# Kernel tuning notes

Measured on AMD Instinct MI355X. Metric: run time of the kernel, lower is better.

The kernel has to match this reference:

```python
import jax, jax.numpy as jnp
import numpy as np

EPS = 1e-5  # torch BatchNorm2d default eps (eval mode with running stats)


def bn(x, g, b, m, v):
    # x: [B,C,H,W]; per-channel affine batchnorm in inference form
    return (x - m[:, None, None]) * (g[:, None, None] / jnp.sqrt(v[:, None, None] + EPS)) + b[:, None, None]


def self_attn(x, Wq, bq, Wk, bk, Wv, bv, rel_h, rel_w):
    # x: [B,C,H,W]; Wq/Wk/Wv: [C,C] (1x1 convs); rel_h: [C,H]; rel_w: [C,W]
    B, C, H, W = x.shape
    N = H * W
    q = jnp.einsum('oc,bchw->bohw', Wq, x).reshape(B, C, N) + bq[None, :, None]
    k = jnp.einsum('oc,bchw->bohw', Wk, x).reshape(B, C, N) + bk[None, :, None]
    v = jnp.einsum('oc,bchw->bohw', Wv, x).reshape(B, C, N) + bv[None, :, None]
    energy = jnp.einsum('bcn,bcm->bnm', q, k)                      # content: Q^T K
    pos = (rel_h[:, :, None] + rel_w[:, None, :]).reshape(C, N)    # [C, H*W]
    energy = energy + jnp.einsum('bcn,cm->bnm', q, pos)            # rel-pos bias term
    attn = jax.nn.softmax(energy, axis=-1)                         # [B,N,N]
    out = jnp.einsum('bcm,bnm->bcn', v, attn)                      # V @ attn^T
    return out.reshape(B, C, H, W)


def conv3x3(x, w):
    return jax.lax.conv_general_dilated(x, w, (1, 1), 'SAME',
                                        dimension_numbers=('NCHW', 'OIHW', 'NCHW'))


def setup_inputs() -> dict:
    key = jax.random.key(0)
    B, C, H, W, NH = 32, 512, 16, 16, 5
    ks = jax.random.split(key, 32)
    f = lambda i, shape, s=1.0: jax.random.normal(ks[i], shape, jnp.float32) * s
    inp = {
        'x0': f(0, (B, C, H, W)), 'x1': f(1, (B, C, H, W)), 'x2': f(2, (B, C, H, W)),
        'x3': f(3, (B, C, H, W)), 'x': f(4, (B, C, H, W)),
        'qW': f(5, (NH, C, C), 0.02), 'qB': f(6, (NH, C), 0.02),
        'kW': f(7, (NH, C, C), 0.02), 'kB': f(8, (NH, C), 0.02),
        'vW': f(9, (NH, C, C), 0.02), 'vB': f(10, (NH, C), 0.02),
        'relH': f(11, (NH, C, H)), 'relW': f(12, (NH, C, W)),
        'msw_W': f(13, (NH - 1, NH * C), 0.02),
        'msw_g': jnp.ones((NH - 1,)), 'msw_b': jnp.zeros((NH - 1,)),
        'msw_m': jnp.zeros((NH - 1,)), 'msw_v': jnp.ones((NH - 1,)),
        'fus_W': f(14, (C, C, 3, 3), 0.02),
        'fus_g': jnp.ones((C,)), 'fus_b': jnp.zeros((C,)),
        'fus_m': jnp.zeros((C,)), 'fus_v': jnp.ones((C,)),
        'top_g': jnp.ones((C,)), 'top_b': jnp.zeros((C,)),
        'top_m': jnp.zeros((C,)), 'top_v': jnp.ones((C,)),
        'h': 16, 'w': 16,
    }
    return inp


def reference(x0, x1, x2, x3, x, qW, qB, kW, kB, vW, vB, relH, relW,
              msw_W, msw_g, msw_b, msw_m, msw_v,
              fus_W, fus_g, fus_b, fus_m, fus_v,
              top_g, top_b, top_m, top_v, h, w):
    B, C, H, W = x.shape
    xs = jnp.stack([x0, x1, x2, x3, x])                            # [5,B,C,H,W]
    outs = jax.vmap(self_attn)(xs, qW, qB, kW, kB, vW, vB, relH, relW)  # [5,B,C,H,W]
    cat = outs.transpose(1, 0, 2, 3, 4).reshape(B, 5 * C, H, W)
    weights = jax.nn.sigmoid(bn(jnp.einsum('oc,bchw->bohw', msw_W, cat),
                                msw_g, msw_b, msw_m, msw_v))        # [B,4,H,W]
    x_ms = (weights[:, 0:1] * outs[0] + weights[:, 1:2] * outs[1]
            + weights[:, 2:3] * outs[2] + weights[:, 3:4] * outs[3] + outs[4])
    x_ms = jax.nn.relu(bn(conv3x3(x_ms, fus_W), fus_g, fus_b, fus_m, fus_v))
    out = jax.nn.relu(bn(x_ms + x, top_g, top_b, top_m, top_v))
    return out
```

## Files before the change

### kernel.cpp

```cpp
#include <hip/hip_runtime.h>
#include <cstdint>

using bf16x8  = __attribute__((ext_vector_type(8))) __bf16;
using f32x4   = __attribute__((ext_vector_type(4))) float;
using ushort8 = __attribute__((ext_vector_type(8))) unsigned short;

#define EPSN 1e-5f

__device__ __forceinline__ void gld16(const void* g, void* l) {
  __builtin_amdgcn_global_load_lds((const __attribute__((address_space(1))) void*)g,
                                   (__attribute__((address_space(3))) void*)l, 16, 0, 0);
}

__device__ __forceinline__ ushort f2bf(float f) {
  __bf16 h = (__bf16)f;
  return __builtin_bit_cast(unsigned short, h);
}
__device__ __forceinline__ float bf2f(ushort u) {
  union { uint32_t u; float f; } v; v.u = ((uint32_t)u) << 16; return v.f;
}

__device__ __forceinline__ void gemm_core(const ushort* __restrict__ Ag,
                                          const ushort* __restrict__ Bg,
                                          int ldk, int ksteps,
                                          ushort* As, ushort* Bs,
                                          f32x4 (&acc)[4][4]) {
  const int t = threadIdx.x, lane = t & 63, w = t >> 6;
  const int wr = w >> 1, wc = w & 1;
  for (int kt = 0; kt < ksteps; ++kt) {
    const int kbase = kt * 64;
#pragma unroll
    for (int p = 0; p < 4; ++p) {
      int q = p * 256 + t;
      int row = q >> 3, slot = q & 7;
      int srcs = slot ^ (row & 7);
      gld16(Ag + (size_t)row * ldk + kbase + srcs * 8, As + (p * 256 + w * 64) * 8);
      gld16(Bg + (size_t)row * ldk + kbase + srcs * 8, Bs + (p * 256 + w * 64) * 8);
    }
    __syncthreads();
#pragma unroll
    for (int kk = 0; kk < 2; ++kk) {
      bf16x8 af[4], bfv[4];
#pragma unroll
      for (int i = 0; i < 4; ++i) {
        int ra = wr * 64 + i * 16 + (lane & 15);
        int sa = (kk * 4 + (lane >> 4)) ^ (ra & 7);
        af[i] = *(const bf16x8*)(As + ra * 64 + sa * 8);
        int rb = wc * 64 + i * 16 + (lane & 15);
        int sb = (kk * 4 + (lane >> 4)) ^ (rb & 7);
        bfv[i] = *(const bf16x8*)(Bs + rb * 64 + sb * 8);
      }
#pragma unroll
      for (int i = 0; i < 4; ++i)
#pragma unroll
        for (int j = 0; j < 4; ++j)
          acc[i][j] = __builtin_amdgcn_mfma_f32_16x16x32_bf16(af[i], bfv[j], acc[i][j], 0, 0, 0);
    }
    __syncthreads();
  }
}

__global__ __launch_bounds__(256) void k_pre(const float* __restrict__ x0,
                                             const float* __restrict__ x1,
                                             const float* __restrict__ x2,
                                             const float* __restrict__ x3,
                                             const float* __restrict__ x4,
                                             const float* __restrict__ qW,
                                             const float* __restrict__ kW,
                                             const float* __restrict__ vW,
                                             const float* __restrict__ relH,
                                             const float* __restrict__ relW,
                                             ushort* __restrict__ xT,
                                             ushort* __restrict__ Wb,
                                             ushort* __restrict__ posb) {
  __shared__ float tile[64][65];
  int bid = blockIdx.x;
  const int t = threadIdx.x;
  if (bid < 5120) {
    const int nt4 = bid & 3;  bid >>= 2;
    const int ct  = bid & 7;  bid >>= 3;
    const int b   = bid & 31; bid >>= 5;
    const int ix  = bid;
    const float* xs = ix == 0 ? x0 : ix == 1 ? x1 : ix == 2 ? x2 : ix == 3 ? x3 : x4;
    const float* src = xs + ((size_t)b * 512 + ct * 64) * 256 + nt4 * 64;
    const int col = t & 63, rq = t >> 6;
#pragma unroll
    for (int rr = 0; rr < 16; ++rr) {
      int row = rr * 4 + rq;
      tile[row][col] = src[(size_t)row * 256 + col];
    }
    __syncthreads();
    ushort* dst = xT + ((size_t)(ix * 32 + b) * 256 + nt4 * 64) * 512 + ct * 64;
#pragma unroll
    for (int rr = 0; rr < 16; ++rr) {
      int nrow = rr * 4 + rq;
      dst[(size_t)nrow * 512 + col] = f2bf(tile[col][nrow]);
    }
  } else if (bid < 8960) {
    int idx = (bid - 5120) * 256 + t;
    int gi = idx * 4;
    int sel = gi / 1310720;
    int off = gi - sel * 1310720;
    const float* src = sel == 0 ? qW : (sel == 1 ? kW : vW);
    float4 vv = *(const float4*)(src + off);
    int h = off / 262144, rest = off - h * 262144;
    ushort4 o;
    o.x = f2bf(vv.x); o.y = f2bf(vv.y); o.z = f2bf(vv.z); o.w = f2bf(vv.w);
    *(ushort4*)(Wb + (size_t)(h * 3 + sel) * 262144 + rest) = o;
  } else {
    int idx8 = (bid - 8960) * 256 + t;
    int e0 = idx8 * 8;
    int c0 = e0 & 511, m = (e0 >> 9) & 255, h = e0 >> 17;
    ushort8 o;
#pragma unroll
    for (int e = 0; e < 8; ++e) {
      int c = c0 + e;
      o[e] = f2bf(relH[((size_t)h * 512 + c) * 16 + (m >> 4)] +
                  relW[((size_t)h * 512 + c) * 16 + (m & 15)]);
    }
    *(ushort8*)(posb + e0) = o;
  }
}

__global__ __launch_bounds__(512, 4) void k_qkv3(const ushort* __restrict__ Wb,
                                                 const ushort* __restrict__ xT,
                                                 const ushort* __restrict__ posb,
                                                 const float* __restrict__ qB,
                                                 const float* __restrict__ kB,
                                                 const float* __restrict__ vB,
                                                 ushort* __restrict__ qT,
                                                 ushort* __restrict__ kpT,
                                                 ushort* __restrict__ vv) {
  extern __shared__ ushort ls[];
  const int t = threadIdx.x, lane = t & 63;
  const int w = t >> 6, wm = w >> 2, wn = w & 3, g = lane >> 4, l = lane & 15;
  int bid = blockIdx.x;
  bid = (bid & 7) * 240 + (bid >> 3);
  const int h = bid / 384;
  const int r = bid % 384;

  const ushort* Ag;
  const ushort* Bg;
  const bool partA = r < 256;
  int pt = 0, nt = 0, mt = 0, ntv = 0;
  if (partA) {
    pt = r >> 2; nt = r & 3;
    Ag = xT + ((size_t)h * 8192 + pt * 128) * 512;
    Bg = Wb + ((size_t)(h * 3 + (nt >> 1)) * 512 + (nt & 1) * 256) * 512;
  } else {
    const int r2 = r - 256;
    mt = r2 >> 5; ntv = r2 & 31;
    Ag = Wb + ((size_t)(h * 3 + 2) * 512 + mt * 128) * 512;
    Bg = xT + ((size_t)h * 8192 + ntv * 256) * 512;
  }

  f32x4 acc[4][4];
#pragma unroll
  for (int i = 0; i < 4; ++i)
#pragma unroll
    for (int j = 0; j < 4; ++j) acc[i][j] = f32x4{0.f, 0.f, 0.f, 0.f};

#define QKV_STAGE(tt, slot)                                                    \
  {                                                                            \
    const int kb_ = (tt) * 32;                                                 \
    ushort* sa_ = ls + (slot) * 4096;                                          \
    ushort* sb_ = ls + 8192 + (slot) * 8192;                                   \
    {                                                                          \
      int q_ = t;                                                              \
      int row_ = q_ >> 2, s4_ = q_ & 3;                                        \
      int src_ = s4_ ^ ((row_ ^ (row_ >> 2)) & 3);                             \
      gld16(Ag + (size_t)row_ * 512 + kb_ + src_ * 8, sa_ + q_ * 8);           \
    }                                                                          \
    _Pragma("unroll")                                                          \
    for (int p_ = 0; p_ < 2; ++p_) {                                           \
      int q_ = p_ * 512 + t;                                                   \
      int row_ = q_ >> 2, s4_ = q_ & 3;                                        \
      int src_ = s4_ ^ ((row_ ^ (row_ >> 2)) & 3);                             \
      gld16(Bg + (size_t)row_ * 512 + kb_ + src_ * 8, sb_ + q_ * 8);           \
    }                                                                          \
  }

#define QKV_COMPUTE(slot)                                                      \
  {                                                                            \
    ushort* sa_ = ls + (slot) * 4096;                                          \
    ushort* sb_ = ls + 8192 + (slot) * 8192;                                   \
    bf16x8 af[4], bfv[4];                                                      \
    _Pragma("unroll")                                                          \
    for (int j_ = 0; j_ < 4; ++j_) {                                           \
      int rb_ = wn * 64 + j_ * 16 + l;                                         \
      int sb2_ = g ^ ((rb_ ^ (rb_ >> 2)) & 3);                                 \
      bfv[j_] = *(const bf16x8*)(sb_ + rb_ * 32 + sb2_ * 8);                   \
    }                                                                          \
    _Pragma("unroll")                                                          \
    for (int i_ = 0; i_ < 4; ++i_) {                                           \
      int ra_ = wm * 64 + i_ * 16 + l;                                         \
      int sa2_ = g ^ ((ra_ ^ (ra_ >> 2)) & 3);                                 \
      af[i_] = *(const bf16x8*)(sa_ + ra_ * 32 + sa2_ * 8);                    \
    }                                                                          \
    asm volatile("s_waitcnt lgkmcnt(0)" ::: "memory");                         \
    __builtin_amdgcn_sched_barrier(0);                                         \
    __builtin_amdgcn_s_setprio(1);                                             \
    _Pragma("unroll")                                                          \
    for (int i_ = 0; i_ < 4; ++i_)                                             \
      _Pragma("unroll")                                                        \
      for (int j_ = 0; j_ < 4; ++j_)                                           \
        acc[i_][j_] = __builtin_amdgcn_mfma_f32_16x16x32_bf16(af[i_], bfv[j_], \
                                                              acc[i_][j_], 0, 0, 0); \
    __builtin_amdgcn_s_setprio(0);                                             \
  }

  QKV_STAGE(0, 0);
  for (int tt = 0; tt < 15; ++tt) {
    __builtin_amdgcn_s_barrier();
    QKV_STAGE(tt + 1, (tt + 1) & 1);
    __builtin_amdgcn_sched_barrier(0);
    asm volatile("s_waitcnt vmcnt(3)" ::: "memory");
    __builtin_amdgcn_s_barrier();
    __builtin_amdgcn_sched_barrier(0);
    QKV_COMPUTE(tt & 1);
  }
  __builtin_amdgcn_sched_barrier(0);
  asm volatile("s_waitcnt vmcnt(0)" ::: "memory");
  __builtin_amdgcn_s_barrier();
  __builtin_amdgcn_sched_barrier(0);
  QKV_COMPUTE(1);
  __syncthreads();

  ushort(*Cs)[260] = (ushort(*)[260])ls;
  if (partA) {
    const bool isq = nt < 2;
    const float* bias = (isq ? qB : kB) + (size_t)h * 512 + (nt & 1) * 256;
    ushort* dst = isq ? qT : kpT;
    float bj[4];
#pragma unroll
    for (int j = 0; j < 4; ++j) bj[j] = bias[wn * 64 + j * 16 + l];
#pragma unroll
    for (int R = 0; R < 2; ++R) {
      if (wm == R) {
#pragma unroll
        for (int i = 0; i < 4; ++i)
#pragma unroll
          for (int j = 0; j < 4; ++j)
#pragma unroll
            for (int rr = 0; rr < 4; ++rr)
              Cs[i * 16 + g * 4 + rr][wn * 64 + j * 16 + l] = f2bf(acc[i][j][rr] + bj[j]);
      }
      __syncthreads();
#pragma unroll
      for (int it = 0; it < 4; ++it) {
        int lin = it * 512 + t;
        int row = lin >> 5, cc8 = (lin & 31) * 8;
        int pglob = pt * 128 + R * 64 + row;
        ushort8 cv = *(const ushort8*)&Cs[row][cc8];
        if (!isq) {
          ushort8 pv = *(const ushort8*)(posb + ((size_t)h * 256 + (pglob & 255)) * 512 +
                                         (nt & 1) * 256 + cc8);
#pragma unroll
          for (int e = 0; e < 8; ++e) cv[e] = f2bf(bf2f(cv[e]) + bf2f(pv[e]));
        }
        *(ushort8*)(dst + ((size_t)h * 8192 + pglob) * 512 + (nt & 1) * 256 + cc8) = cv;
      }
      if (R == 0) __syncthreads();
    }
  } else {
    const float* bias = vB + (size_t)h * 512 + mt * 128;
#pragma unroll
    for (int R = 0; R < 2; ++R) {
      if (wm == R) {
#pragma unroll
        for (int i = 0; i < 4; ++i) {
          float4 b4 = *(const float4*)(bias + R * 64 + i * 16 + g * 4);
#pragma unroll
          for (int j = 0; j < 4; ++j)
#pragma unroll
            for (int rr = 0; rr < 4; ++rr)
              Cs[i * 16 + g * 4 + rr][wn * 64 + j * 16 + l] =
                  f2bf(acc[i][j][rr] + ((const float*)&b4)[rr]);
        }
      }
      __syncthreads();
#pragma unroll
      for (int it = 0; it < 4; ++it) {
        int lin = it * 512 + t;
        int row = lin >> 5, cc8 = (lin & 31) * 8;
        int og = mt * 128 + R * 64 + row;
        ushort8 cv = *(const ushort8*)&Cs[row][cc8];
        *(ushort8*)(vv + (((size_t)(h * 32 + ntv)) * 512 + og) * 256 + cc8) = cv;
      }
      if (R == 0) __syncthreads();
    }
  }
#undef QKV_STAGE
#undef QKV_COMPUTE
}

__global__ __launch_bounds__(256) void k_attn(const ushort* __restrict__ qT,
                                              const ushort* __restrict__ kpT,
                                              const float* __restrict__ fusW,
                                              ushort* __restrict__ attn,
                                              ushort* __restrict__ Wconv) {
  __shared__ ushort sm[20480];
  __shared__ float red[4][64];
  __shared__ float comb[64];
  int bid = blockIdx.x;
  const int t = threadIdx.x;
  if (bid >= 640) {
    int p = (bid - 640) * 256 + t;
    const float* src = fusW + (size_t)p * 9;
    float vv[9];
#pragma unroll
    for (int s = 0; s < 9; ++s) vv[s] = src[s];
#pragma unroll
    for (int s = 0; s < 9; ++s) Wconv[(size_t)s * 262144 + p] = f2bf(vv[s]);
    return;
  }
  bid = (bid & 7) * 80 + (bid >> 3);
  const int rt = bid & 3;
  const int hb = bid >> 2;
  ushort* As = sm;
  ushort* Bs = sm + 4096;
  const ushort* Ag = qT + ((size_t)hb * 256 + rt * 64) * 512;
  const ushort* Bg = kpT + (size_t)hb * 256 * 512;
  const int lane = t & 63, w = t >> 6, g = lane >> 4, l = lane & 15;

  f32x4 acc[4][4];
#pragma unroll
  for (int i = 0; i < 4; ++i)
#pragma unroll
    for (int j = 0; j < 4; ++j) acc[i][j] = f32x4{0.f, 0.f, 0.f, 0.f};

  for (int kt = 0; kt < 8; ++kt) {
    const int kbase = kt * 64;
#pragma unroll
    for (int p = 0; p < 2; ++p) {
      int q = p * 256 + t;
      int row = q >> 3, slot = q & 7, srcs = slot ^ (row & 7);
      gld16(Ag + (size_t)row * 512 + kbase + srcs * 8, As + (p * 256 + w * 64) * 8);
    }
#pragma unroll
    for (int p = 0; p < 8; ++p) {
      int q = p * 256 + t;
      int row = q >> 3, slot = q & 7, srcs = slot ^ (row & 7);
      gld16(Bg + (size_t)row * 512 + kbase + srcs * 8, Bs + (p * 256 + w * 64) * 8);
    }
    __syncthreads();
#pragma unroll
    for (int kk = 0; kk < 2; ++kk) {
      bf16x8 af[4], bfv[4];
#pragma unroll
      for (int i = 0; i < 4; ++i) {
        int ra = i * 16 + l;
        int sa = (kk * 4 + g) ^ (ra & 7);
        af[i] = *(const bf16x8*)(As + ra * 64 + sa * 8);
        int rb = w * 64 + i * 16 + l;
        int sb = (kk * 4 + g) ^ (rb & 7);
        bfv[i] = *(const bf16x8*)(Bs + rb * 64 + sb * 8);
      }
#pragma unroll
      for (int i = 0; i < 4; ++i)
#pragma unroll
        for (int j = 0; j < 4; ++j)
          acc[i][j] = __builtin_amdgcn_mfma_f32_16x16x32_bf16(af[i], bfv[j], acc[i][j], 0, 0, 0);
    }
    __syncthreads();
  }

#pragma unroll
  for (int i = 0; i < 4; ++i)
#pragma unroll
    for (int rr = 0; rr < 4; ++rr) {
      float v = fmaxf(fmaxf(acc[i][0][rr], acc[i][1][rr]), fmaxf(acc[i][2][rr], acc[i][3][rr]));
#pragma unroll
      for (int m = 1; m < 16; m <<= 1) v = fmaxf(v, __shfl_xor(v, m));
      if (l == 0) red[w][i * 16 + g * 4 + rr] = v;
    }
  __syncthreads();
  if (t < 64) comb[t] = fmaxf(fmaxf(red[0][t], red[1][t]), fmaxf(red[2][t], red[3][t]));
  __syncthreads();
#pragma unroll
  for (int i = 0; i < 4; ++i)
#pragma unroll
    for (int rr = 0; rr < 4; ++rr) {
      float mx = comb[i * 16 + g * 4 + rr];
      float s = 0.f;
#pragma unroll
      for (int j = 0; j < 4; ++j) {
        float e = expf(acc[i][j][rr] - mx);
        acc[i][j][rr] = e;
        s += e;
      }
#pragma unroll
      for (int m = 1; m < 16; m <<= 1) s += __shfl_xor(s, m);
      if (l == 0) red[w][i * 16 + g * 4 + rr] = s;
    }
  __syncthreads();
  if (t < 64) comb[t] = red[0][t] + red[1][t] + red[2][t] + red[3][t];
  __syncthreads();
  ushort(*P)[260] = (ushort(*)[260])sm;
#pragma unroll
  for (int i = 0; i < 4; ++i)
#pragma unroll
    for (int rr = 0; rr < 4; ++rr) {
      int row = i * 16 + g * 4 + rr;
      float inv = 1.f / comb[row];
#pragma unroll
      for (int j = 0; j < 4; ++j)
        P[row][w * 64 + j * 16 + l] = f2bf(acc[i][j][rr] * inv);
    }
  __syncthreads();
  ushort* Arow = attn + (size_t)hb * 65536 + (size_t)rt * 16384;
#pragma unroll
  for (int it = 0; it < 8; ++it) {
    int lin = it * 256 + t;
    int row = lin >> 5, c8 = (lin & 31) * 8;
    ushort8 cv = *(const ushort8*)&P[row][c8];
    *(ushort8*)(Arow + (size_t)row * 256 + c8) = cv;
  }
}

__global__ __launch_bounds__(256) void k_pv(const ushort* __restrict__ attn,
                                            const ushort* __restrict__ vv,
                                            ushort* __restrict__ OT) {
  __shared__ ushort lds[128 * 148];
  ushort* As = lds;
  ushort* Bs = lds + 8192;
  int bid = blockIdx.x;
  bid = (bid & 7) * 160 + (bid >> 3);
  const int nt = bid & 3; bid >>= 2;
  const int mt = bid & 1; bid >>= 1;
  const size_t hb = (size_t)bid;
  const ushort* Ag = attn + (hb * 256 + mt * 128) * 256;
  const ushort* Bg = vv + (hb * 512 + nt * 128) * 256;
  f32x4 acc[4][4];
#pragma unroll
  for (int i = 0; i < 4; ++i)
#pragma unroll
    for (int j = 0; j < 4; ++j) acc[i][j] = f32x4{0.f, 0.f, 0.f, 0.f};
  gemm_core(Ag, Bg, 256, 4, As, Bs, acc);
  const int t = threadIdx.x, lane = t & 63, w = t >> 6;
  const int wr = w >> 1, wc = w & 1, g = lane >> 4, l = lane & 15;
  ushort(*Cs)[148] = (ushort(*)[148])lds;
#pragma unroll
  for (int i = 0; i < 4; ++i)
#pragma unroll
    for (int j = 0; j < 4; ++j)
#pragma unroll
      for (int rr = 0; rr < 4; ++rr)
        Cs[wr * 64 + i * 16 + g * 4 + rr][wc * 64 + j * 16 + l] = f2bf(acc[i][j][rr]);
  __syncthreads();
#pragma unroll
  for (int it = 0; it < 8; ++it) {
    int lin = it * 256 + t;
    int row = lin >> 4, cc = (lin & 15) * 8;
    ushort8 cv = *(const ushort8*)&Cs[row][cc];
    *(ushort8*)(OT + (hb * 256 + mt * 128 + row) * 512 + nt * 128 + cc) = cv;
  }
}

__global__ __launch_bounds__(256) void k_weights(const ushort* __restrict__ OT,
                                                 const float* __restrict__ mswW,
                                                 const float* __restrict__ mg,
                                                 const float* __restrict__ mb,
                                                 const float* __restrict__ mm,
                                                 const float* __restrict__ mv,
                                                 ushort* __restrict__ xmsT) {
  __shared__ float msw[10240];
  const int t = threadIdx.x, lane = t & 63, w = t >> 6;
#pragma unroll
  for (int it = 0; it < 10; ++it) {
    int idx = it * 1024 + t * 4;
    *(float4*)(msw + idx) = *(const float4*)(mswW + idx);
  }
  __syncthreads();
  const size_t pix = (size_t)blockIdx.x * 4 + w;
  float o[5][2][4];
#pragma unroll
  for (int h = 0; h < 5; ++h)
#pragma unroll
    for (int hf = 0; hf < 2; ++hf) {
      ushort4 v = *(const ushort4*)(OT + ((size_t)h * 8192 + pix) * 512 + hf * 256 + lane * 4);
      o[h][hf][0] = bf2f(v.x); o[h][hf][1] = bf2f(v.y);
      o[h][hf][2] = bf2f(v.z); o[h][hf][3] = bf2f(v.w);
    }
  float a[4] = {0.f, 0.f, 0.f, 0.f};
#pragma unroll
  for (int j = 0; j < 4; ++j)
#pragma unroll
    for (int h = 0; h < 5; ++h)
#pragma unroll
      for (int hf = 0; hf < 2; ++hf) {
        float4 m4 = *(const float4*)(msw + j * 2560 + h * 512 + hf * 256 + lane * 4);
        a[j] += m4.x * o[h][hf][0] + m4.y * o[h][hf][1] +
                m4.z * o[h][hf][2] + m4.w * o[h][hf][3];
      }
#pragma unroll
  for (int m = 1; m < 64; m <<= 1) {
    a[0] += __shfl_xor(a[0], m); a[1] += __shfl_xor(a[1], m);
    a[2] += __shfl_xor(a[2], m); a[3] += __shfl_xor(a[3], m);
  }
  float wj[4];
#pragma unroll
  for (int j = 0; j < 4; ++j) {
    float val = (a[j] - mm[j]) * (mg[j] * rsqrtf(mv[j] + EPSN)) + mb[j];
    wj[j] = 1.f / (1.f + expf(-val));
  }
#pragma unroll
  for (int hf = 0; hf < 2; ++hf) {
    float r0 = wj[0] * o[0][hf][0] + wj[1] * o[1][hf][0] + wj[2] * o[2][hf][0] + wj[3] * o[3][hf][0] + o[4][hf][0];
    float r1 = wj[0] * o[0][hf][1] + wj[1] * o[1][hf][1] + wj[2] * o[2][hf][1] + wj[3] * o[3][hf][1] + o[4][hf][1];
    float r2 = wj[0] * o[0][hf][2] + wj[1] * o[1][hf][2] + wj[2] * o[2][hf][2] + wj[3] * o[3][hf][2] + o[4][hf][2];
    float r3 = wj[0] * o[0][hf][3] + wj[1] * o[1][hf][3] + wj[2] * o[2][hf][3] + wj[3] * o[3][hf][3] + o[4][hf][3];
    ushort4 pk; pk.x = f2bf(r0); pk.y = f2bf(r1); pk.z = f2bf(r2); pk.w = f2bf(r3);
    *(ushort4*)(xmsT + pix * 512 + hf * 256 + lane * 4) = pk;
  }
}

__global__ __launch_bounds__(256) void k_conv(const ushort* __restrict__ Wconv,
                                              const ushort* __restrict__ xmsT,
                                              float* __restrict__ y1a,
                                              float* __restrict__ y1b) {
  __shared__ ushort As3[3 * 128 * 64];
  __shared__ ushort xp[180 * 76];
  int bid = blockIdx.x;
  bid = (bid & 7) * 64 + (bid >> 3);
  const int ntl = bid & 1; bid >>= 1;
  const int mt = bid & 3;  bid >>= 2;
  const int halfk = bid & 1; bid >>= 1;
  const int bb = bid;
  const int y0 = ntl * 8;
  const int t = threadIdx.x, lane = t & 63, w = t >> 6, wr = w >> 1, wc = w & 1;
  f32x4 acc[4][4];
#pragma unroll
  for (int i = 0; i < 4; ++i)
#pragma unroll
    for (int j = 0; j < 4; ++j) acc[i][j] = f32x4{0.f, 0.f, 0.f, 0.f};

  for (int cb = halfk * 4; cb < halfk * 4 + 4; ++cb) {
    __syncthreads();
    for (int u = t; u < 1440; u += 256) {
      int slot = u & 7;
      int xpi = (u >> 3) % 18;
      int rl = u / 144;
      int yg = y0 - 1 + rl, xg = xpi - 1;
      uint4 val = make_uint4(0, 0, 0, 0);
      if (yg >= 0 && yg < 16 && (unsigned)xg < 16u)
        val = *(const uint4*)(xmsT + ((size_t)bb * 256 + yg * 16 + xg) * 512 + cb * 64 + slot * 8);
      *(uint4*)(xp + (rl * 18 + xpi) * 76 + slot * 8) = val;
    }
    for (int dy = 0; dy < 3; ++dy) {
#pragma unroll
      for (int dx = 0; dx < 3; ++dx)
#pragma unroll
        for (int p = 0; p < 4; ++p) {
          int q = p * 256 + t;
          int row = q >> 3, slot = q & 7, srcs = slot ^ (row & 7);
          gld16(Wconv + ((size_t)(dy * 3 + dx) * 512 + mt * 128 + row) * 512 + cb * 64 + srcs * 8,
                As3 + dx * 8192 + (p * 256 + w * 64) * 8);
        }
      __syncthreads();
#pragma unroll
      for (int dx = 0; dx < 3; ++dx)
#pragma unroll
        for (int kk = 0; kk < 2; ++kk) {
          bf16x8 af[4], bfv[4];
#pragma unroll
          for (int i = 0; i < 4; ++i) {
            int ra = wr * 64 + i * 16 + (lane & 15);
            int sa = (kk * 4 + (lane >> 4)) ^ (ra & 7);
            af[i] = *(const bf16x8*)(As3 + dx * 8192 + ra * 64 + sa * 8);
            int nl = wc * 64 + i * 16 + (lane & 15);
            int pp = ((nl >> 4) + dy) * 18 + (nl & 15) + dx;
            bfv[i] = *(const bf16x8*)(xp + pp * 76 + (kk * 4 + (lane >> 4)) * 8);
          }
#pragma unroll
          for (int i = 0; i < 4; ++i)
#pragma unroll
            for (int j = 0; j < 4; ++j)
              acc[i][j] = __builtin_amdgcn_mfma_f32_16x16x32_bf16(af[i], bfv[j], acc[i][j], 0, 0, 0);
        }
      __syncthreads();
    }
  }
  float* yp = halfk ? y1b : y1a;
  const int o0 = mt * 128 + wr * 64 + ((lane >> 4) << 2);
  const int n0 = ntl * 128 + wc * 64 + (lane & 15);
#pragma unroll
  for (int i = 0; i < 4; ++i)
#pragma unroll
    for (int j = 0; j < 4; ++j)
#pragma unroll
      for (int rr = 0; rr < 4; ++rr) {
        int o = o0 + i * 16 + rr, n = n0 + j * 16;
        yp[((size_t)bb * 512 + o) * 256 + n] = acc[i][j][rr];
      }
}

__global__ __launch_bounds__(256) void k_top(const float* __restrict__ y1a,
                                             const float* __restrict__ y1b,
                                             const float* __restrict__ x,
                                             const float* __restrict__ fg,
                                             const float* __restrict__ fb,
                                             const float* __restrict__ fm,
                                             const float* __restrict__ fv,
                                             const float* __restrict__ tg,
                                             const float* __restrict__ tb,
                                             const float* __restrict__ tm,
                                             const float* __restrict__ tv,
                                             float* __restrict__ out) {
  size_t i4 = ((size_t)blockIdx.x * 256 + threadIdx.x) * 4;
  int c = (int)((i4 >> 8) & 511);
  float4 a = *(const float4*)(y1a + i4);
  float4 bq = *(const float4*)(y1b + i4);
  float4 xx = *(const float4*)(x + i4);
  float sf = fg[c] * rsqrtf(fv[c] + EPSN), mf = fm[c], bf_ = fb[c];
  float st = tg[c] * rsqrtf(tv[c] + EPSN), mt_ = tm[c], bt_ = tb[c];
  float4 o;
  float v;
  v = fmaxf((a.x + bq.x - mf) * sf + bf_, 0.f); o.x = fmaxf((v + xx.x - mt_) * st + bt_, 0.f);
  v = fmaxf((a.y + bq.y - mf) * sf + bf_, 0.f); o.y = fmaxf((v + xx.y - mt_) * st + bt_, 0.f);
  v = fmaxf((a.z + bq.z - mf) * sf + bf_, 0.f); o.z = fmaxf((v + xx.z - mt_) * st + bt_, 0.f);
  v = fmaxf((a.w + bq.w - mf) * sf + bf_, 0.f); o.w = fmaxf((v + xx.w - mt_) * st + bt_, 0.f);
  *(float4*)(out + i4) = o;
}

extern "C" void kernel_launch(void* const* d_in, const int* in_sizes, int n_in,
                              void* d_out, int out_size, void* d_ws, size_t ws_size,
                              hipStream_t stream) {
  const float* x0   = (const float*)d_in[0];
  const float* x1   = (const float*)d_in[1];
  const float* x2   = (const float*)d_in[2];
  const float* x3   = (const float*)d_in[3];
  const float* x4   = (const float*)d_in[4];
  const float* qW   = (const float*)d_in[5];
  const float* qB   = (const float*)d_in[6];
  const float* kW   = (const float*)d_in[7];
  const float* kB   = (const float*)d_in[8];
  const float* vW   = (const float*)d_in[9];
  const float* vB   = (const float*)d_in[10];
  const float* relH = (const float*)d_in[11];
  const float* relW = (const float*)d_in[12];
  const float* mswW = (const float*)d_in[13];
  const float* msg  = (const float*)d_in[14];
  const float* msb  = (const float*)d_in[15];
  const float* msm  = (const float*)d_in[16];
  const float* msv  = (const float*)d_in[17];
  const float* fusW = (const float*)d_in[18];
  const float* fg   = (const float*)d_in[19];
  const float* fb   = (const float*)d_in[20];
  const float* fm   = (const float*)d_in[21];
  const float* fv   = (const float*)d_in[22];
  const float* tg   = (const float*)d_in[23];
  const float* tb   = (const float*)d_in[24];
  const float* tm   = (const float*)d_in[25];
  const float* tv   = (const float*)d_in[26];

  if (ws_size < 180355072ull) return;
  char* ws = (char*)d_ws;
  ushort* xT    = (ushort*)(ws + 0);
  ushort* attn  = (ushort*)(ws + 0);
  ushort* Wconv = (ushort*)(ws + 20971520);
  ushort* qT    = (ushort*)(ws + 41943040);
  ushort* xmsT  = (ushort*)(ws + 41943040);
  float*  y1a   = (float*)(ws + 50331648);
  float*  y1b   = (float*)(ws + 67108864);
  ushort* kpT   = (ushort*)(ws + 83886080);
  ushort* OT    = (ushort*)(ws + 83886080);
  ushort* vv    = (ushort*)(ws + 125829120);
  ushort* Wb    = (ushort*)(ws + 167772160);
  ushort* posb  = (ushort*)(ws + 175636480);

  k_pre    <<<9280, 256, 0, stream>>>(x0, x1, x2, x3, x4, qW, kW, vW, relH, relW,
                                      xT, Wb, posb);
  k_qkv3   <<<1920, 512, 49152, stream>>>(Wb, xT, posb, qB, kB, vB, qT, kpT, vv);
  k_attn   <<<1664, 256, 0, stream>>>(qT, kpT, fusW, attn, Wconv);
  k_pv     <<<1280, 256, 0, stream>>>(attn, vv, OT);
  k_weights<<<2048, 256, 0, stream>>>(OT, mswW, msg, msb, msm, msv, xmsT);
  k_conv   <<<512,  256, 0, stream>>>(Wconv, xmsT, y1a, y1b);
  k_top    <<<4096, 256, 0, stream>>>(y1a, y1b, x4, fg, fb, fm, fv, tg, tb, tm, tv, (float*)d_out);
}
```

Before: 256.1 us.

## Triple-buffer QKV and PV GEMMs, fuse conv epilogue with BN/residual, drop split-K

The QKV GEMM moves from a double-buffered to a triple-buffered LDS pipeline, using more dynamic shared memory and prefetching two stages ahead. The PV GEMM drops the shared synchronous gemm_core for the same triple-buffered pipeline with 32-wide k steps and raised MFMA priority. The 3x3 conv no longer splits K across blocks. It runs with 512 threads and applies both batchnorms, ReLUs and the residual in its epilogue from precomputed per-channel scale/shift, which removes the k_top kernel and the fp32 partial buffers. The trade-off is half as many conv blocks, 256 instead of 512, which may leave compute units idle, plus strided scalar output stores.

Result: faster. 249.0 us (-2.8%).

```diff
diff --git a/kernel.cpp b/kernel.cpp
--- a/kernel.cpp
+++ b/kernel.cpp
@@ -18,46 +18,6 @@
 }
 __device__ __forceinline__ float bf2f(ushort u) {
   union { uint32_t u; float f; } v; v.u = ((uint32_t)u) << 16; return v.f;
-}
-
-__device__ __forceinline__ void gemm_core(const ushort* __restrict__ Ag,
-                                          const ushort* __restrict__ Bg,
-                                          int ldk, int ksteps,
-                                          ushort* As, ushort* Bs,
-                                          f32x4 (&acc)[4][4]) {
-  const int t = threadIdx.x, lane = t & 63, w = t >> 6;
-  const int wr = w >> 1, wc = w & 1;
-  for (int kt = 0; kt < ksteps; ++kt) {
-    const int kbase = kt * 64;
-#pragma unroll
-    for (int p = 0; p < 4; ++p) {
-      int q = p * 256 + t;
-      int row = q >> 3, slot = q & 7;
-      int srcs = slot ^ (row & 7);
-      gld16(Ag + (size_t)row * ldk + kbase + srcs * 8, As + (p * 256 + w * 64) * 8);
-      gld16(Bg + (size_t)row * ldk + kbase + srcs * 8, Bs + (p * 256 + w * 64) * 8);
-    }
-    __syncthreads();
-#pragma unroll
-    for (int kk = 0; kk < 2; ++kk) {
-      bf16x8 af[4], bfv[4];
-#pragma unroll
-      for (int i = 0; i < 4; ++i) {
-        int ra = wr * 64 + i * 16 + (lane & 15);
-        int sa = (kk * 4 + (lane >> 4)) ^ (ra & 7);
-        af[i] = *(const bf16x8*)(As + ra * 64 + sa * 8);
-        int rb = wc * 64 + i * 16 + (lane & 15);
-        int sb = (kk * 4 + (lane >> 4)) ^ (rb & 7);
-        bfv[i] = *(const bf16x8*)(Bs + rb * 64 + sb * 8);
-      }
-#pragma unroll
-      for (int i = 0; i < 4; ++i)
-#pragma unroll
-        for (int j = 0; j < 4; ++j)
-          acc[i][j] = __builtin_amdgcn_mfma_f32_16x16x32_bf16(af[i], bfv[j], acc[i][j], 0, 0, 0);
-    }
-    __syncthreads();
-  }
 }
 
 __global__ __launch_bounds__(256) void k_pre(const float* __restrict__ x0,
@@ -70,9 +30,18 @@
                                              const float* __restrict__ vW,
                                              const float* __restrict__ relH,
                                              const float* __restrict__ relW,
+                                             const float* __restrict__ fg,
+                                             const float* __restrict__ fb,
+                                             const float* __restrict__ fm,
+                                             const float* __restrict__ fv,
+                                             const float* __restrict__ tg,
+                                             const float* __restrict__ tb,
+                                             const float* __restrict__ tm,
+                                             const float* __restrict__ tv,
                                              ushort* __restrict__ xT,
                                              ushort* __restrict__ Wb,
-                                             ushort* __restrict__ posb) {
+                                             ushort* __restrict__ posb,
+                                             float4* __restrict__ bnp) {
   __shared__ float tile[64][65];
   int bid = blockIdx.x;
   const int t = threadIdx.x;
@@ -107,7 +76,7 @@
     ushort4 o;
     o.x = f2bf(vv.x); o.y = f2bf(vv.y); o.z = f2bf(vv.z); o.w = f2bf(vv.w);
     *(ushort4*)(Wb + (size_t)(h * 3 + sel) * 262144 + rest) = o;
-  } else {
+  } else if (bid < 9280) {
     int idx8 = (bid - 8960) * 256 + t;
     int e0 = idx8 * 8;
     int c0 = e0 & 511, m = (e0 >> 9) & 255, h = e0 >> 17;
@@ -119,6 +88,13 @@
                   relW[((size_t)h * 512 + c) * 16 + (m & 15)]);
     }
     *(ushort8*)(posb + e0) = o;
+  } else {
+    int o = (bid - 9280) * 256 + t;
+    float sf = fg[o] * rsqrtf(fv[o] + EPSN);
+    float c1 = fb[o] - fm[o] * sf;
+    float st = tg[o] * rsqrtf(tv[o] + EPSN);
+    float c2 = tb[o] - tm[o] * st;
+    bnp[o] = make_float4(sf, c1, st, c2);
   }
 }
 
@@ -164,7 +140,7 @@
   {                                                                            \
     const int kb_ = (tt) * 32;                                                 \
     ushort* sa_ = ls + (slot) * 4096;                                          \
-    ushort* sb_ = ls + 8192 + (slot) * 8192;                                   \
+    ushort* sb_ = ls + 12288 + (slot) * 8192;                                  \
     {                                                                          \
       int q_ = t;                                                              \
       int row_ = q_ >> 2, s4_ = q_ & 3;                                        \
@@ -183,7 +159,7 @@
 #define QKV_COMPUTE(slot)                                                      \
   {                                                                            \
     ushort* sa_ = ls + (slot) * 4096;                                          \
-    ushort* sb_ = ls + 8192 + (slot) * 8192;                                   \
+    ushort* sb_ = ls + 12288 + (slot) * 8192;                                  \
     bf16x8 af[4], bfv[4];                                                      \
     _Pragma("unroll")                                                          \
     for (int j_ = 0; j_ < 4; ++j_) {                                           \
@@ -210,20 +186,18 @@
   }
 
   QKV_STAGE(0, 0);
-  for (int tt = 0; tt < 15; ++tt) {
+  QKV_STAGE(1, 1);
+  for (int tt = 0; tt < 16; ++tt) {
     __builtin_amdgcn_s_barrier();
-    QKV_STAGE(tt + 1, (tt + 1) & 1);
+    if (tt < 14) { QKV_STAGE(tt + 2, (tt + 2) % 3); }
     __builtin_amdgcn_sched_barrier(0);
-    asm volatile("s_waitcnt vmcnt(3)" ::: "memory");
+    if (tt < 14)       asm volatile("s_waitcnt vmcnt(6)" ::: "memory");
+    else if (tt == 14) asm volatile("s_waitcnt vmcnt(3)" ::: "memory");
+    else               asm volatile("s_waitcnt vmcnt(0)" ::: "memory");
     __builtin_amdgcn_s_barrier();
     __builtin_amdgcn_sched_barrier(0);
-    QKV_COMPUTE(tt & 1);
-  }
-  __builtin_amdgcn_sched_barrier(0);
-  asm volatile("s_waitcnt vmcnt(0)" ::: "memory");
-  __builtin_amdgcn_s_barrier();
-  __builtin_amdgcn_sched_barrier(0);
-  QKV_COMPUTE(1);
+    QKV_COMPUTE(tt % 3);
+  }
   __syncthreads();
 
   ushort(*Cs)[260] = (ushort(*)[260])ls;
@@ -421,9 +395,9 @@
 __global__ __launch_bounds__(256) void k_pv(const ushort* __restrict__ attn,
                                             const ushort* __restrict__ vv,
                                             ushort* __restrict__ OT) {
-  __shared__ ushort lds[128 * 148];
-  ushort* As = lds;
-  ushort* Bs = lds + 8192;
+  __shared__ ushort pls[24576];
+  const int t = threadIdx.x, lane = t & 63, w = t >> 6;
+  const int wr = w >> 1, wc = w & 1, g = lane >> 4, l = lane & 15;
   int bid = blockIdx.x;
   bid = (bid & 7) * 160 + (bid >> 3);
   const int nt = bid & 3; bid >>= 2;
@@ -431,15 +405,70 @@
   const size_t hb = (size_t)bid;
   const ushort* Ag = attn + (hb * 256 + mt * 128) * 256;
   const ushort* Bg = vv + (hb * 512 + nt * 128) * 256;
+
   f32x4 acc[4][4];
 #pragma unroll
   for (int i = 0; i < 4; ++i)
 #pragma unroll
     for (int j = 0; j < 4; ++j) acc[i][j] = f32x4{0.f, 0.f, 0.f, 0.f};
-  gemm_core(Ag, Bg, 256, 4, As, Bs, acc);
-  const int t = threadIdx.x, lane = t & 63, w = t >> 6;
-  const int wr = w >> 1, wc = w & 1, g = lane >> 4, l = lane & 15;
-  ushort(*Cs)[148] = (ushort(*)[148])lds;
+
+#define PV_STAGE(tt, slot)                                                     \
+  {                                                                            \
+    const int kb_ = (tt) * 32;                                                 \
+    ushort* sa_ = pls + (slot) * 4096;                                         \
+    ushort* sb_ = pls + 12288 + (slot) * 4096;                                 \
+    _Pragma("unroll")                                                          \
+    for (int p_ = 0; p_ < 2; ++p_) {                                           \
+      int q_ = p_ * 256 + t;                                                   \
+      int row_ = q_ >> 2, s4_ = q_ & 3;                                        \
+      int src_ = s4_ ^ ((row_ ^ (row_ >> 2)) & 3);                             \
+      gld16(Ag + (size_t)row_ * 256 + kb_ + src_ * 8, sa_ + q_ * 8);           \
+      gld16(Bg + (size_t)row_ * 256 + kb_ + src_ * 8, sb_ + q_ * 8);           \
+    }                                                                          \
+  }
+
+#define PV_COMPUTE(slot)                                                       \
+  {                                                                            \
+    ushort* sa_ = pls + (slot) * 4096;                                         \
+    ushort* sb_ = pls + 12288 + (slot) * 4096;                                 \
+    bf16x8 af[4], bfv[4];                                                      \
+    _Pragma("unroll")                                                          \
+    for (int i_ = 0; i_ < 4; ++i_) {                                           \
+      int ra_ = wr * 64 + i_ * 16 + l;                                         \
+      int sa2_ = g ^ ((ra_ ^ (ra_ >> 2)) & 3);                                 \
+      af[i_] = *(const bf16x8*)(sa_ + ra_ * 32 + sa2_ * 8);                    \
+      int rb_ = wc * 64 + i_ * 16 + l;                                         \
+      int sb2_ = g ^ ((rb_ ^ (rb_ >> 2)) & 3);                                 \
+      bfv[i_] = *(const bf16x8*)(sb_ + rb_ * 32 + sb2_ * 8);                   \
+    }                                                                          \
+    asm volatile("s_waitcnt lgkmcnt(0)" ::: "memory");                         \
+    __builtin_amdgcn_sched_barrier(0);                                         \
+    __builtin_amdgcn_s_setprio(1);                                             \
+    _Pragma("unroll")                                                          \
+    for (int i_ = 0; i_ < 4; ++i_)                                             \
+      _Pragma("unroll")                                                        \
+      for (int j_ = 0; j_ < 4; ++j_)                                           \
+        acc[i_][j_] = __builtin_amdgcn_mfma_f32_16x16x32_bf16(af[i_], bfv[j_], \
+                                                              acc[i_][j_], 0, 0, 0); \
+    __builtin_amdgcn_s_setprio(0);                                             \
+  }
+
+  PV_STAGE(0, 0);
+  PV_STAGE(1, 1);
+  for (int tt = 0; tt < 8; ++tt) {
+    __builtin_amdgcn_s_barrier();
+    if (tt < 6) { PV_STAGE(tt + 2, (tt + 2) % 3); }
+    __builtin_amdgcn_sched_barrier(0);
+    if (tt < 6)       asm volatile("s_waitcnt vmcnt(8)" ::: "memory");
+    else if (tt == 6) asm volatile("s_waitcnt vmcnt(4)" ::: "memory");
+    else              asm volatile("s_waitcnt vmcnt(0)" ::: "memory");
+    __builtin_amdgcn_s_barrier();
+    __builtin_amdgcn_sched_barrier(0);
+    PV_COMPUTE(tt % 3);
+  }
+  __syncthreads();
+
+  ushort(*Cs)[148] = (ushort(*)[148])pls;
 #pragma unroll
   for (int i = 0; i < 4; ++i)
 #pragma unroll
@@ -455,6 +484,8 @@
     ushort8 cv = *(const ushort8*)&Cs[row][cc];
     *(ushort8*)(OT + (hb * 256 + mt * 128 + row) * 512 + nt * 128 + cc) = cv;
   }
+#undef PV_STAGE
+#undef PV_COMPUTE
 }
 
 __global__ __launch_bounds__(256) void k_weights(const ushort* __restrict__ OT,
@@ -515,29 +546,30 @@
   }
 }
 
-__global__ __launch_bounds__(256) void k_conv(const ushort* __restrict__ Wconv,
+__global__ __launch_bounds__(512) void k_conv(const ushort* __restrict__ Wconv,
                                               const ushort* __restrict__ xmsT,
-                                              float* __restrict__ y1a,
-                                              float* __restrict__ y1b) {
-  __shared__ ushort As3[3 * 128 * 64];
+                                              const float* __restrict__ x,
+                                              const float4* __restrict__ bnp,
+                                              float* __restrict__ out) {
+  __shared__ ushort As3[3 * 8192];
   __shared__ ushort xp[180 * 76];
   int bid = blockIdx.x;
-  bid = (bid & 7) * 64 + (bid >> 3);
+  bid = (bid & 7) * 32 + (bid >> 3);
   const int ntl = bid & 1; bid >>= 1;
   const int mt = bid & 3;  bid >>= 2;
-  const int halfk = bid & 1; bid >>= 1;
   const int bb = bid;
   const int y0 = ntl * 8;
-  const int t = threadIdx.x, lane = t & 63, w = t >> 6, wr = w >> 1, wc = w & 1;
-  f32x4 acc[4][4];
-#pragma unroll
-  for (int i = 0; i < 4; ++i)
-#pragma unroll
-    for (int j = 0; j < 4; ++j) acc[i][j] = f32x4{0.f, 0.f, 0.f, 0.f};
-
-  for (int cb = halfk * 4; cb < halfk * 4 + 4; ++cb) {
+  const int t = threadIdx.x, lane = t & 63;
+  const int w = t >> 6, wm = w >> 2, wn = w & 3, g = lane >> 4, l = lane & 15;
+  f32x4 acc[4][2];
+#pragma unroll
+  for (int i = 0; i < 4; ++i)
+#pragma unroll
+    for (int j = 0; j < 2; ++j) acc[i][j] = f32x4{0.f, 0.f, 0.f, 0.f};
+
+  for (int cb = 0; cb < 8; ++cb) {
     __syncthreads();
-    for (int u = t; u < 1440; u += 256) {
+    for (int u = t; u < 1440; u += 512) {
       int slot = u & 7;
       int xpi = (u >> 3) % 18;
       int rl = u / 144;
@@ -551,76 +583,54 @@
 #pragma unroll
       for (int dx = 0; dx < 3; ++dx)
 #pragma unroll
-        for (int p = 0; p < 4; ++p) {
-          int q = p * 256 + t;
+        for (int p = 0; p < 2; ++p) {
+          int q = p * 512 + t;
           int row = q >> 3, slot = q & 7, srcs = slot ^ (row & 7);
           gld16(Wconv + ((size_t)(dy * 3 + dx) * 512 + mt * 128 + row) * 512 + cb * 64 + srcs * 8,
-                As3 + dx * 8192 + (p * 256 + w * 64) * 8);
+                As3 + dx * 8192 + q * 8);
         }
       __syncthreads();
 #pragma unroll
       for (int dx = 0; dx < 3; ++dx)
 #pragma unroll
         for (int kk = 0; kk < 2; ++kk) {
-          bf16x8 af[4], bfv[4];
+          bf16x8 af[4], bfv[2];
+#pragma unroll
+          for (int j = 0; j < 2; ++j) {
+            int nl = wn * 32 + j * 16 + l;
+            int pp = ((nl >> 4) + dy) * 18 + (nl & 15) + dx;
+            bfv[j] = *(const bf16x8*)(xp + pp * 76 + (kk * 4 + g) * 8);
+          }
 #pragma unroll
           for (int i = 0; i < 4; ++i) {
-            int ra = wr * 64 + i * 16 + (lane & 15);
-            int sa = (kk * 4 + (lane >> 4)) ^ (ra & 7);
+            int ra = wm * 64 + i * 16 + l;
+            int sa = (kk * 4 + g) ^ (ra & 7);
             af[i] = *(const bf16x8*)(As3 + dx * 8192 + ra * 64 + sa * 8);
-            int nl = wc * 64 + i * 16 + (lane & 15);
-            int pp = ((nl >> 4) + dy) * 18 + (nl & 15) + dx;
-            bfv[i] = *(const bf16x8*)(xp + pp * 76 + (kk * 4 + (lane >> 4)) * 8);
           }
 #pragma unroll
           for (int i = 0; i < 4; ++i)
 #pragma unroll
-            for (int j = 0; j < 4; ++j)
+            for (int j = 0; j < 2; ++j)
               acc[i][j] = __builtin_amdgcn_mfma_f32_16x16x32_bf16(af[i], bfv[j], acc[i][j], 0, 0, 0);
         }
       __syncthreads();
     }
   }
-  float* yp = halfk ? y1b : y1a;
-  const int o0 = mt * 128 + wr * 64 + ((lane >> 4) << 2);
-  const int n0 = ntl * 128 + wc * 64 + (lane & 15);
-#pragma unroll
-  for (int i = 0; i < 4; ++i)
-#pragma unroll
-    for (int j = 0; j < 4; ++j)
-#pragma unroll
-      for (int rr = 0; rr < 4; ++rr) {
-        int o = o0 + i * 16 + rr, n = n0 + j * 16;
-        yp[((size_t)bb * 512 + o) * 256 + n] = acc[i][j][rr];
-      }
-}
-
-__global__ __launch_bounds__(256) void k_top(const float* __restrict__ y1a,
-                                             const float* __restrict__ y1b,
-                                             const float* __restrict__ x,
-                                             const float* __restrict__ fg,
-                                             const float* __restrict__ fb,
-                                             const float* __restrict__ fm,
-                                             const float* __restrict__ fv,
-                                             const float* __restrict__ tg,
-                                             const float* __restrict__ tb,
-                                             const float* __restrict__ tm,
-                                             const float* __restrict__ tv,
-                                             float* __restrict__ out) {
-  size_t i4 = ((size_t)blockIdx.x * 256 + threadIdx.x) * 4;
-  int c = (int)((i4 >> 8) & 511);
-  float4 a = *(const float4*)(y1a + i4);
-  float4 bq = *(const float4*)(y1b + i4);
-  float4 xx = *(const float4*)(x + i4);
-  float sf = fg[c] * rsqrtf(fv[c] + EPSN), mf = fm[c], bf_ = fb[c];
-  float st = tg[c] * rsqrtf(tv[c] + EPSN), mt_ = tm[c], bt_ = tb[c];
-  float4 o;
-  float v;
-  v = fmaxf((a.x + bq.x - mf) * sf + bf_, 0.f); o.x = fmaxf((v + xx.x - mt_) * st + bt_, 0.f);
-  v = fmaxf((a.y + bq.y - mf) * sf + bf_, 0.f); o.y = fmaxf((v + xx.y - mt_) * st + bt_, 0.f);
-  v = fmaxf((a.z + bq.z - mf) * sf + bf_, 0.f); o.z = fmaxf((v + xx.z - mt_) * st + bt_, 0.f);
-  v = fmaxf((a.w + bq.w - mf) * sf + bf_, 0.f); o.w = fmaxf((v + xx.w - mt_) * st + bt_, 0.f);
-  *(float4*)(out + i4) = o;
+  const int o0 = mt * 128 + wm * 64;
+#pragma unroll
+  for (int i = 0; i < 4; ++i)
+#pragma unroll
+    for (int rr = 0; rr < 4; ++rr) {
+      int o = o0 + i * 16 + g * 4 + rr;
+      float4 p4 = bnp[o];
+#pragma unroll
+      for (int j = 0; j < 2; ++j) {
+        int n = ntl * 128 + wn * 32 + j * 16 + l;
+        size_t idx = ((size_t)bb * 512 + o) * 256 + n;
+        float z = fmaxf(acc[i][j][rr] * p4.x + p4.y, 0.f);
+        out[idx] = fmaxf((z + x[idx]) * p4.z + p4.w, 0.f);
+      }
+    }
 }
 
 extern "C" void kernel_launch(void* const* d_in, const int* in_sizes, int n_in,
@@ -661,20 +671,22 @@
   ushort* Wconv = (ushort*)(ws + 20971520);
   ushort* qT    = (ushort*)(ws + 41943040);
   ushort* xmsT  = (ushort*)(ws + 41943040);
-  float*  y1a   = (float*)(ws + 50331648);
-  float*  y1b   = (float*)(ws + 67108864);
   ushort* kpT   = (ushort*)(ws + 83886080);
   ushort* OT    = (ushort*)(ws + 83886080);
   ushort* vv    = (ushort*)(ws + 125829120);
   ushort* Wb    = (ushort*)(ws + 167772160);
   ushort* posb  = (ushort*)(ws + 175636480);
-
-  k_pre    <<<9280, 256, 0, stream>>>(x0, x1, x2, x3, x4, qW, kW, vW, relH, relW,
-                                      xT, Wb, posb);
-  k_qkv3   <<<1920, 512, 49152, stream>>>(Wb, xT, posb, qB, kB, vB, qT, kpT, vv);
+  float4* bnp   = (float4*)(ws + 176947200);
+
+  hipFuncSetAttribute((const void*)k_qkv3,
+                      hipFuncAttributeMaxDynamicSharedMemorySize, 73728);
+
+  k_pre    <<<9282, 256, 0, stream>>>(x0, x1, x2, x3, x4, qW, kW, vW, relH, relW,
+                                      fg, fb, fm, fv, tg, tb, tm, tv,
+                                      xT, Wb, posb, (float4*)bnp);
+  k_qkv3   <<<1920, 512, 73728, stream>>>(Wb, xT, posb, qB, kB, vB, qT, kpT, vv);
   k_attn   <<<1664, 256, 0, stream>>>(qT, kpT, fusW, attn, Wconv);
   k_pv     <<<1280, 256, 0, stream>>>(attn, vv, OT);
   k_weights<<<2048, 256, 0, stream>>>(OT, mswW, msg, msb, msm, msv, xmsT);
-  k_conv   <<<512,  256, 0, stream>>>(Wconv, xmsT, y1a, y1b);
-  k_top    <<<4096, 256, 0, stream>>>(y1a, y1b, x4, fg, fb, fm, fv, tg, tb, tm, tv, (float*)d_out);
-}
+  k_conv   <<<256,  512, 0, stream>>>(Wconv, xmsT, x4, bnp, (float*)d_out);
+}
```
